# Optimization experiments

Hardware: AMD Instinct MI355X
Metric: run time of the kernel (lower is better)

## Reference

```python
import jax, jax.numpy as jnp
import numpy as np

B, L, ENC, EMB, H, V = 64, 33, 512, 256, 512, 32000


def setup_inputs() -> dict:
    key = jax.random.key(0)
    ks = jax.random.split(key, 16)
    x = jax.random.normal(ks[0], (B, ENC), dtype=jnp.float32)
    padded_target = jax.random.randint(ks[1], (B, L), 0, V)
    target_lengths = jax.random.randint(ks[2], (B,), 2, L + 1)
    target_lengths = target_lengths.at[0].set(L)  # pin max length -> static step count
    s = 0.05
    return {
        "x": x,
        "padded_target": padded_target,
        "target_lengths": target_lengths,
        "embed": jax.random.normal(ks[3], (V, EMB), dtype=jnp.float32) * s,
        "W_h0": jax.random.normal(ks[4], (H, ENC), dtype=jnp.float32) * s,
        "b_h0": jnp.zeros((H,), jnp.float32),
        "W_c0": jax.random.normal(ks[5], (H, ENC), dtype=jnp.float32) * s,
        "b_c0": jnp.zeros((H,), jnp.float32),
        "W_ih": jax.random.normal(ks[6], (4 * H, ENC + EMB), dtype=jnp.float32) * s,
        "W_hh": jax.random.normal(ks[7], (4 * H, H), dtype=jnp.float32) * s,
        "b_ih": jnp.zeros((4 * H,), jnp.float32),
        "b_hh": jnp.zeros((4 * H,), jnp.float32),
        "W_out": jax.random.normal(ks[8], (V, H), dtype=jnp.float32) * s,
        "b_out": jnp.zeros((V,), jnp.float32),
    }


def reference(x, padded_target, target_lengths, embed, W_h0, b_h0, W_c0, b_c0,
              W_ih, W_hh, b_ih, b_hh, W_out, b_out):
    # sort by length, descending (packed-sequence ordering)
    sorted_indices = jnp.argsort(-target_lengths)
    x = x[sorted_indices]                      # [B, ENC]
    tgt = padded_target[sorted_indices]        # [B, L]
    lens = target_lengths[sorted_indices] - 1  # decode steps per row
    emb = embed[tgt]                           # [B, L, EMB]

    h = x @ W_h0.T + b_h0                      # context-initialized state
    c = x @ W_c0.T + b_c0
    T = padded_target.shape[1] - 1             # static max steps (max len pinned to L)

    def step(carry, inp):
        h, c = carry
        e_t, t = inp
        active = (lens > t)[:, None]           # rows still decoding (prefix, sorted)
        g = jnp.concatenate([x, e_t], axis=1) @ W_ih.T + b_ih + h @ W_hh.T + b_hh
        i, f, gg, o = jnp.split(g, 4, axis=1)  # torch LSTMCell gate order i,f,g,o
        c_new = jax.nn.sigmoid(f) * c + jax.nn.sigmoid(i) * jnp.tanh(gg)
        h_new = jax.nn.sigmoid(o) * jnp.tanh(c_new)
        h = jnp.where(active, h_new, h)        # inactive rows keep frozen state
        c = jnp.where(active, c_new, c)
        pred = jnp.where(active, h_new @ W_out.T + b_out, 0.0)  # dropout p=0
        return (h, c), pred

    (_, _), preds = jax.lax.scan(
        step, (h, c), (jnp.transpose(emb[:, :T], (1, 0, 2)), jnp.arange(T)))
    prediction = jnp.transpose(preds, (1, 0, 2))  # [B, T, V]
    return prediction, sorted_indices
```

## Files before the change

kernel.cpp:

```cpp
#include <hip/hip_runtime.h>

typedef __attribute__((ext_vector_type(8))) short short8;
typedef __attribute__((ext_vector_type(8))) unsigned short ushort8;
typedef __attribute__((ext_vector_type(4))) float f32x4;

#define DEV __device__ __forceinline__

DEV unsigned short f2bf(float f) {
  unsigned int u = __float_as_uint(f);
  u += 0x7fffu + ((u >> 16) & 1u);
  return (unsigned short)(u >> 16);
}
DEV float sigm(float x) { return 1.f / (1.f + __expf(-x)); }
DEV float tanh_(float x) { return 1.f - 2.f / (1.f + __expf(2.f * x)); }

typedef __attribute__((address_space(1))) const void* as1cv;
typedef __attribute__((address_space(3))) void* as3v;
DEV void gll16(const void* g, void* l) {
  __builtin_amdgcn_global_load_lds((as1cv)g, (as3v)l, 16, 0, 0);
}

__global__ void __launch_bounds__(256) k_pre(const float* __restrict__ x,
    const int* __restrict__ ptar, const int* __restrict__ tlen,
    const float* __restrict__ W_h0, const float* __restrict__ W_c0,
    const float* __restrict__ W_ih, const float* __restrict__ W_hh,
    int* __restrict__ sidx, int* __restrict__ lens, int* __restrict__ base,
    int* __restrict__ inv, int* __restrict__ Pw, int* __restrict__ tok,
    unsigned short* __restrict__ xsb, float* __restrict__ tail,
    unsigned short* __restrict__ Wpro, unsigned short* __restrict__ Wihb2,
    unsigned short* __restrict__ Whb) {
  int bid = blockIdx.x, tid = threadIdx.x;
  if (bid > 0) {
    long long g = (long long)(bid - 1) * 2048 + tid * 8;
    const float* src;
    unsigned short* dst;
    if (g < 262144) {
      src = W_h0 + g; dst = Wpro + g;
    } else if (g < 524288) {
      long long l = g - 262144; src = W_c0 + l; dst = Wpro + 262144 + l;
    } else if (g < 1572864) {
      long long l = g - 524288;
      long long r = l >> 9, c = l & 511;
      src = W_ih + r * 768 + c; dst = Wpro + 524288 + l;
    } else if (g < 2097152) {
      long long l = g - 1572864;
      long long r = l >> 8, c = l & 255;
      src = W_ih + r * 768 + 512 + c; dst = Wihb2 + l;
    } else {
      long long l = g - 2097152; src = W_hh + l; dst = Whb + l;
    }
    float4 v0 = *(const float4*)src, v1 = *(const float4*)(src + 4);
    ushort8 o;
    o[0] = f2bf(v0.x); o[1] = f2bf(v0.y); o[2] = f2bf(v0.z); o[3] = f2bf(v0.w);
    o[4] = f2bf(v1.x); o[5] = f2bf(v1.y); o[6] = f2bf(v1.z); o[7] = f2bf(v1.w);
    *(ushort8*)dst = o;
    return;
  }
  __shared__ int ss[64], ls[64], bs[64];
  if (tid < 64) {
    int li = tlen[tid];
    int rank = 0;
    for (int j = 0; j < 64; ++j) {
      int lj = tlen[j];
      rank += (lj > li || (lj == li && j < tid)) ? 1 : 0;
    }
    ss[rank] = tid;
  }
  __syncthreads();
  if (tid < 64) {
    int src = ss[tid];
    sidx[tid] = src;
    int l = tlen[src] - 1;
    ls[tid] = l;
    lens[tid] = l;
    tail[tid] = (float)src;
  }
  __syncthreads();
  if (tid == 0) {
    int s = 0;
    for (int b = 0; b < 64; ++b) { bs[b] = s; base[b] = s; s += ls[b]; }
    Pw[0] = s;
  }
  __syncthreads();
  for (int idx = tid; idx < 2048; idx += 256) {
    int b = idx >> 5, t = idx & 31;
    if (t < ls[b]) inv[bs[b] + t] = idx;
  }
  for (int idx = tid; idx < 32 * 64; idx += 256) {
    int t = idx >> 6, b = idx & 63;
    tok[idx] = ptar[ss[b] * 33 + t];
  }
  for (int idx = tid; idx < 64 * 512; idx += 256) {
    int b = idx >> 9;
    xsb[idx] = f2bf(x[ss[b] * 512 + (idx & 511)]);
  }
}

__global__ void __launch_bounds__(256) k_mid(const unsigned short* __restrict__ xsb,
    const unsigned short* __restrict__ Wpro, const float* __restrict__ b_h0,
    const float* __restrict__ b_c0, const float* __restrict__ b_ih,
    const float* __restrict__ b_hh, unsigned short* __restrict__ h0b,
    float* __restrict__ c, float* __restrict__ gx,
    const int* __restrict__ tok, const float* __restrict__ embed,
    unsigned short* __restrict__ Eb) {
  int bid = blockIdx.x, tid = threadIdx.x;
  if (bid >= 48) {
    int gid = (bid - 48) * 256 + tid;
    int row = gid >> 5, c8 = (gid & 31) * 8;
    const float* src = embed + (size_t)tok[row] * 256 + c8;
    float4 v0 = *(const float4*)src, v1 = *(const float4*)(src + 4);
    ushort8 o;
    o[0] = f2bf(v0.x); o[1] = f2bf(v0.y); o[2] = f2bf(v0.z); o[3] = f2bf(v0.w);
    o[4] = f2bf(v1.x); o[5] = f2bf(v1.y); o[6] = f2bf(v1.z); o[7] = f2bf(v1.w);
    *(ushort8*)(Eb + (size_t)row * 256 + c8) = o;
    return;
  }
  int lane = tid & 63, w = tid >> 6;
  int n0 = bid * 64 + w * 16;
  int lr = lane & 15, lk = lane >> 4;
  f32x4 acc[4];
#pragma unroll
  for (int i = 0; i < 4; ++i) acc[i] = (f32x4){0.f, 0.f, 0.f, 0.f};
  const unsigned short* B = Wpro + (size_t)(n0 + lr) * 512 + lk * 8;
  const unsigned short* A = xsb + (size_t)lr * 512 + lk * 8;
#pragma unroll
  for (int ks = 0; ks < 16; ++ks) {
    short8 bfr = *(const short8*)(B + ks * 32);
#pragma unroll
    for (int mi = 0; mi < 4; ++mi) {
      short8 af = *(const short8*)(A + mi * 16 * 512 + ks * 32);
      acc[mi] = __builtin_amdgcn_mfma_f32_16x16x32_bf16(af, bfr, acc[mi], 0, 0, 0);
    }
  }
  int n = n0 + lr;
#pragma unroll
  for (int mi = 0; mi < 4; ++mi)
#pragma unroll
    for (int r = 0; r < 4; ++r) {
      int b = mi * 16 + lk * 4 + r;
      float v = acc[mi][r];
      if (n < 512) {
        h0b[b * 512 + n] = f2bf(v + b_h0[n]);
      } else if (n < 1024) {
        int u = n - 512;
        c[b * 512 + u] = v + b_c0[u];
      } else {
        int j = n - 1024;
        gx[(size_t)b * 2048 + j] = v + b_ih[j] + b_hh[j];
      }
    }
}

__global__ void __launch_bounds__(256) k_ga2(const unsigned short* __restrict__ Eb,
    const unsigned short* __restrict__ Wb2, const float* __restrict__ gx,
    float* __restrict__ GA, const float* __restrict__ W_out,
    unsigned short* __restrict__ Wob) {
  int bid = blockIdx.x, tid = threadIdx.x;
  if (bid >= 256) {
    long long basei = (long long)(bid - 256) * 65536;
#pragma unroll 4
    for (int it = 0; it < 32; ++it) {
      long long i = basei + (long long)it * 2048 + tid * 8;
      float4 v0 = *(const float4*)(W_out + i);
      float4 v1 = *(const float4*)(W_out + i + 4);
      ushort8 o;
      o[0] = f2bf(v0.x); o[1] = f2bf(v0.y); o[2] = f2bf(v0.z); o[3] = f2bf(v0.w);
      o[4] = f2bf(v1.x); o[5] = f2bf(v1.y); o[6] = f2bf(v1.z); o[7] = f2bf(v1.w);
      *(ushort8*)(Wob + i) = o;
    }
    return;
  }
  __shared__ alignas(16) char ldsbuf[32768];
  char* ldsA = ldsbuf;
  char* ldsB = ldsbuf + 16384;
  int mt = bid & 15, nt = bid >> 4;
  int m0 = mt * 128, n0 = nt * 128;
  int lane = tid & 63, w = tid >> 6;
  int wm = w >> 1, wn = w & 1;
  f32x4 acc[4][4];
#pragma unroll
  for (int a = 0; a < 4; ++a)
#pragma unroll
    for (int bq = 0; bq < 4; ++bq) acc[a][bq] = (f32x4){0.f, 0.f, 0.f, 0.f};
  const unsigned short* Arow = Eb + (size_t)m0 * 256;
  const unsigned short* Brow = Wb2 + (size_t)n0 * 256;
  for (int kt = 0; kt < 4; ++kt) {
    int k0 = kt * 64;
    if (kt) __syncthreads();
#pragma unroll
    for (int j = 0; j < 4; ++j) {
      int ci = j * 256 + w * 64 + lane;
      int r = ci >> 3;
      int clog = ((ci & 7) << 4) ^ ((r & 7) << 4);
      int ldst = (j * 256 + w * 64) * 16;
      gll16((const char*)(Arow + (size_t)r * 256 + k0) + clog, ldsA + ldst);
      gll16((const char*)(Brow + (size_t)r * 256 + k0) + clog, ldsB + ldst);
    }
    __syncthreads();
#pragma unroll
    for (int kk = 0; kk < 2; ++kk) {
      short8 af[4], bf[4];
      int cb = kk * 64 + (lane >> 4) * 16;
#pragma unroll
      for (int i = 0; i < 4; ++i) {
        int ar = wm * 64 + i * 16 + (lane & 15);
        af[i] = *(const short8*)(ldsA + ar * 128 + (cb ^ ((ar & 7) << 4)));
        int br = wn * 64 + i * 16 + (lane & 15);
        bf[i] = *(const short8*)(ldsB + br * 128 + (cb ^ ((br & 7) << 4)));
      }
#pragma unroll
      for (int mi = 0; mi < 4; ++mi)
#pragma unroll
        for (int ni = 0; ni < 4; ++ni)
          acc[mi][ni] = __builtin_amdgcn_mfma_f32_16x16x32_bf16(
              af[mi], bf[ni], acc[mi][ni], 0, 0, 0);
    }
  }
#pragma unroll
  for (int mi = 0; mi < 4; ++mi) {
    int mb = m0 + wm * 64 + mi * 16 + ((lane >> 4) << 2);
#pragma unroll
    for (int r = 0; r < 4; ++r) {
      int m = mb + r;
#pragma unroll
      for (int ni = 0; ni < 4; ++ni) {
        int j = n0 + wn * 64 + ni * 16 + (lane & 15);
        GA[(size_t)m * 2048 + j] = acc[mi][ni][r] + gx[(size_t)(m & 63) * 2048 + j];
      }
    }
  }
}

__global__ void __launch_bounds__(256, 1) k_step4(
    const unsigned short* __restrict__ hin, unsigned short* __restrict__ hout,
    float* __restrict__ c, const float* __restrict__ GA,
    const unsigned short* __restrict__ Whb, const int* __restrict__ lens,
    const int* __restrict__ base, unsigned short* __restrict__ Hm, int t) {
  int tid = threadIdx.x, bid = blockIdx.x;
  int mq = bid & 3, ug = bid >> 2;
  int r0 = mq * 16;
  if (t > lens[r0]) return;
  int lane = tid & 63, w = tid >> 6;
  int lr = lane & 15, lk = lane >> 4;
  int gate = lr >> 2, ul = lr & 3;
  int u = ug * 16 + w * 4 + ul;

  const float* gab = GA + ((size_t)t * 64 + r0) * 2048 + gate * 512 + u;
  float gv[4];
#pragma unroll
  for (int r = 0; r < 4; ++r) gv[r] = gab[(size_t)(lk * 4 + r) * 2048];

  const unsigned short* Bp = Whb + ((size_t)gate * 512 + u) * 512 + lk * 8;
  const unsigned short* Ap = hin + (size_t)(r0 + lr) * 512 + lk * 8;
  short8 bfr[16], afr[16];
#pragma unroll
  for (int ks = 0; ks < 16; ++ks) bfr[ks] = *(const short8*)(Bp + ks * 32);
#pragma unroll
  for (int ks = 0; ks < 16; ++ks) afr[ks] = *(const short8*)(Ap + ks * 32);
  f32x4 acc = (f32x4){0.f, 0.f, 0.f, 0.f};
#pragma unroll
  for (int ks = 0; ks < 16; ++ks)
    acc = __builtin_amdgcn_mfma_f32_16x16x32_bf16(afr[ks], bfr[ks], acc, 0, 0, 0);

#pragma unroll
  for (int r = 0; r < 4; ++r) {
    float v = acc[r] + gv[r];
    float av = (gate == 2) ? tanh_(v) : sigm(v);
    float x4 = __shfl_xor(av, 4);
    float x8 = __shfl_xor(av, 8);
    float x12 = __shfl_xor(av, 12);
    float vi = (gate == 0) ? av : (gate == 1) ? x4 : (gate == 2) ? x8 : x12;
    float vf = (gate == 1) ? av : (gate == 0) ? x4 : (gate == 3) ? x8 : x12;
    float vg = (gate == 2) ? av : (gate == 3) ? x4 : (gate == 0) ? x8 : x12;
    float vo = (gate == 3) ? av : (gate == 2) ? x4 : (gate == 1) ? x8 : x12;
    if (gate == 0) {
      int b = r0 + lk * 4 + r;
      float cold = c[b * 512 + u];
      float cn = vf * cold + vi * vg;
      float hn = vo * tanh_(cn);
      bool act = lens[b] > t;
      if (act) c[b * 512 + u] = cn;
      unsigned short hbv = f2bf(hn);
      hout[b * 512 + u] = act ? hbv : hin[b * 512 + u];
      if (act) Hm[((size_t)(base[b] + t)) * 512 + u] = hbv;
    }
  }
}

__global__ void __launch_bounds__(512) k_gemm(const unsigned short* __restrict__ Hm,
    const unsigned short* __restrict__ Wb, const float* __restrict__ b_out,
    const int* __restrict__ inv, const int* __restrict__ Pw,
    const int* __restrict__ lens, float* __restrict__ out) {
  int bid = blockIdx.x, tid = threadIdx.x;
  if (bid >= 2000) {
    int idx = bid - 2000;
    float4 z = {0.f, 0.f, 0.f, 0.f};
#pragma unroll
    for (int k = 0; k < 4; ++k) {
      int m = idx * 4 + k;
      int b = m >> 5, t = m & 31;
      if (lens[b] > t) continue;
      float* row = out + (size_t)m * 32000;
      for (int i = tid * 4; i < 32000; i += 2048) *(float4*)(row + i) = z;
    }
    return;
  }
  __shared__ alignas(16) char ldsbuf[49152];
  char* ldsA = ldsbuf;
  char* ldsB = ldsbuf + 16384;
  int P = Pw[0];
  int sb = (bid & 7) * 250 + (bid >> 3);
  int mt = sb % 16, nt = sb / 16;
  int m0 = mt * 128, n0 = nt * 256;
  if (m0 >= P) return;
  int lane = tid & 63, w = tid >> 6;
  int wm = w >> 2, wn = w & 3;
  f32x4 acc[4][4];
#pragma unroll
  for (int a = 0; a < 4; ++a)
#pragma unroll
    for (int bq = 0; bq < 4; ++bq) acc[a][bq] = (f32x4){0.f, 0.f, 0.f, 0.f};
  const unsigned short* Arow = Hm + (size_t)m0 * 512;
  const unsigned short* Brow = Wb + (size_t)n0 * 512;
  for (int kt = 0; kt < 8; ++kt) {
    int k0 = kt * 64;
    if (kt) __syncthreads();
#pragma unroll
    for (int j = 0; j < 2; ++j) {
      int ci = j * 512 + tid;
      int r = ci >> 3;
      int clog = ((ci & 7) << 4) ^ ((r & 7) << 4);
      gll16((const char*)(Arow + (size_t)r * 512 + k0) + clog, ldsA + ci * 16);
    }
#pragma unroll
    for (int j = 0; j < 4; ++j) {
      int ci = j * 512 + tid;
      int r = ci >> 3;
      int clog = ((ci & 7) << 4) ^ ((r & 7) << 4);
      gll16((const char*)(Brow + (size_t)r * 512 + k0) + clog, ldsB + ci * 16);
    }
    __syncthreads();
#pragma unroll
    for (int kk = 0; kk < 2; ++kk) {
      short8 af[4], bf[4];
      int cb = kk * 64 + (lane >> 4) * 16;
#pragma unroll
      for (int i = 0; i < 4; ++i) {
        int ar = wm * 64 + i * 16 + (lane & 15);
        af[i] = *(const short8*)(ldsA + ar * 128 + (cb ^ ((ar & 7) << 4)));
        int br = wn * 64 + i * 16 + (lane & 15);
        bf[i] = *(const short8*)(ldsB + br * 128 + (cb ^ ((br & 7) << 4)));
      }
#pragma unroll
      for (int mi = 0; mi < 4; ++mi)
#pragma unroll
        for (int ni = 0; ni < 4; ++ni)
          acc[mi][ni] = __builtin_amdgcn_mfma_f32_16x16x32_bf16(
              af[mi], bf[ni], acc[mi][ni], 0, 0, 0);
    }
  }
#pragma unroll
  for (int mi = 0; mi < 4; ++mi) {
    int pb = m0 + wm * 64 + mi * 16 + ((lane >> 4) << 2);
#pragma unroll
    for (int r = 0; r < 4; ++r) {
      int p = pb + r;
      if (p >= P) continue;
      size_t orow = (size_t)inv[p] * 32000;
#pragma unroll
      for (int ni = 0; ni < 4; ++ni) {
        int n = n0 + wn * 64 + ni * 16 + (lane & 15);
        out[orow + n] = acc[mi][ni][r] + b_out[n];
      }
    }
  }
}

extern "C" void kernel_launch(void* const* d_in, const int* in_sizes, int n_in,
                              void* d_out, int out_size, void* d_ws, size_t ws_size,
                              hipStream_t stream) {
  const float* x     = (const float*)d_in[0];
  const int*   ptar  = (const int*)d_in[1];
  const int*   tlen  = (const int*)d_in[2];
  const float* embed = (const float*)d_in[3];
  const float* W_h0  = (const float*)d_in[4];
  const float* b_h0  = (const float*)d_in[5];
  const float* W_c0  = (const float*)d_in[6];
  const float* b_c0  = (const float*)d_in[7];
  const float* W_ih  = (const float*)d_in[8];
  const float* W_hh  = (const float*)d_in[9];
  const float* b_ih  = (const float*)d_in[10];
  const float* b_hh  = (const float*)d_in[11];
  const float* W_out = (const float*)d_in[12];
  const float* b_out = (const float*)d_in[13];
  float* out = (float*)d_out;

  char* ws = (char*)d_ws;
  size_t off = 0;
  auto alloc = [&](size_t bytes) {
    void* p = ws + off;
    off += (bytes + 255) & ~(size_t)255;
    return p;
  };
  unsigned short* Wob = (unsigned short*)alloc(32000ull * 512 * 2);
  unsigned short* Hm  = (unsigned short*)alloc(2048ull * 512 * 2);
  unsigned short* h0b = (unsigned short*)alloc(64 * 512 * 2);
  unsigned short* h1b = (unsigned short*)alloc(64 * 512 * 2);
  float* cbuf = (float*)alloc(64 * 512 * 4);
  float* gx   = (float*)alloc(64 * 2048 * 4);
  int* sidx = (int*)alloc(64 * 4);
  int* lens = (int*)alloc(64 * 4);
  int* base = (int*)alloc(64 * 4);
  int* inv  = (int*)alloc(2048 * 4);
  int* Pw   = (int*)alloc(4);
  int* tok  = (int*)alloc(2048 * 4);

  float* GA = out;
  unsigned short* Wpro  = (unsigned short*)(out + 4194304);
  unsigned short* Wihb2 = (unsigned short*)(out + 4980736);
  unsigned short* Whb   = (unsigned short*)(out + 5242880);
  unsigned short* Eb    = (unsigned short*)(out + 5767168);
  unsigned short* xsb   = (unsigned short*)(out + 6029312);
  float* tail = out + 65536000;

  k_pre<<<1537, 256, 0, stream>>>(x, ptar, tlen, W_h0, W_c0, W_ih, W_hh,
                                  sidx, lens, base, inv, Pw, tok, xsb, tail,
                                  Wpro, Wihb2, Whb);
  k_mid<<<304, 256, 0, stream>>>(xsb, Wpro, b_h0, b_c0, b_ih, b_hh, h0b, cbuf,
                                 gx, tok, embed, Eb);
  k_ga2<<<506, 256, 0, stream>>>(Eb, Wihb2, gx, GA, W_out, Wob);

  unsigned short* hb[2] = {h0b, h1b};
  for (int t = 0; t < 32; ++t)
    k_step4<<<128, 256, 0, stream>>>(hb[t & 1], hb[(t + 1) & 1], cbuf, GA, Whb,
                                     lens, base, Hm, t);

  k_gemm<<<2512, 512, 0, stream>>>(Hm, Wob, b_out, inv, Pw, lens, out);
  (void)in_sizes; (void)n_in; (void)out_size; (void)ws_size;
}
```

Baseline: 433.3 us.

## Fuse LSTM step launches into persistent kernel with global atomic barriers

Replaces the 32 per-timestep k_step4 launches with one persistent k_steps kernel that keeps W_hh fragments, cell state and the previous h in registers. Blocks in the same 16-row group synchronise each step through an atomic counter barrier, with h exchanged through cache-bypassing loads and stores. The next step's gate inputs are prefetched, and the W_out bf16 conversion moves from k_ga2 into extra blocks of the step kernel so it overlaps the serial recurrence. The barrier depends on all 32 blocks of a row group being co-resident, which is a deadlock risk, and the spin loop can contend with the conversion blocks for bandwidth.

```diff
diff --git a/kernel.cpp b/kernel.cpp
--- a/kernel.cpp
+++ b/kernel.cpp
@@ -18,6 +18,18 @@
 typedef __attribute__((address_space(3))) void* as3v;
 DEV void gll16(const void* g, void* l) {
   __builtin_amdgcn_global_load_lds((as1cv)g, (as3v)l, 16, 0, 0);
+}
+
+DEV void st2_llc(unsigned short* p, unsigned short v) {
+  unsigned int vv = v;
+  asm volatile("global_store_short %0, %1, off sc0 sc1" :: "v"(p), "v"(vv)
+               : "memory");
+}
+DEV short8 ld16_llc(const unsigned short* p) {
+  short8 r;
+  asm volatile("global_load_dwordx4 %0, %1, off sc0 sc1" : "=&v"(r) : "v"(p)
+               : "memory");
+  return r;
 }
 
 __global__ void __launch_bounds__(256) k_pre(const float* __restrict__ x,
@@ -28,7 +40,7 @@
     int* __restrict__ inv, int* __restrict__ Pw, int* __restrict__ tok,
     unsigned short* __restrict__ xsb, float* __restrict__ tail,
     unsigned short* __restrict__ Wpro, unsigned short* __restrict__ Wihb2,
-    unsigned short* __restrict__ Whb) {
+    unsigned short* __restrict__ Whb, int* __restrict__ bar) {
   int bid = blockIdx.x, tid = threadIdx.x;
   if (bid > 0) {
     long long g = (long long)(bid - 1) * 2048 + tid * 8;
@@ -57,6 +69,7 @@
     return;
   }
   __shared__ int ss[64], ls[64], bs[64];
+  for (int idx = tid; idx < 2048; idx += 256) bar[idx] = 0;
   if (tid < 64) {
     int li = tlen[tid];
     int rank = 0;
@@ -153,26 +166,11 @@
 
 __global__ void __launch_bounds__(256) k_ga2(const unsigned short* __restrict__ Eb,
     const unsigned short* __restrict__ Wb2, const float* __restrict__ gx,
-    float* __restrict__ GA, const float* __restrict__ W_out,
-    unsigned short* __restrict__ Wob) {
-  int bid = blockIdx.x, tid = threadIdx.x;
-  if (bid >= 256) {
-    long long basei = (long long)(bid - 256) * 65536;
-#pragma unroll 4
-    for (int it = 0; it < 32; ++it) {
-      long long i = basei + (long long)it * 2048 + tid * 8;
-      float4 v0 = *(const float4*)(W_out + i);
-      float4 v1 = *(const float4*)(W_out + i + 4);
-      ushort8 o;
-      o[0] = f2bf(v0.x); o[1] = f2bf(v0.y); o[2] = f2bf(v0.z); o[3] = f2bf(v0.w);
-      o[4] = f2bf(v1.x); o[5] = f2bf(v1.y); o[6] = f2bf(v1.z); o[7] = f2bf(v1.w);
-      *(ushort8*)(Wob + i) = o;
-    }
-    return;
-  }
+    float* __restrict__ GA) {
   __shared__ alignas(16) char ldsbuf[32768];
   char* ldsA = ldsbuf;
   char* ldsB = ldsbuf + 16384;
+  int bid = blockIdx.x, tid = threadIdx.x;
   int mt = bid & 15, nt = bid >> 4;
   int m0 = mt * 128, n0 = nt * 128;
   int lane = tid & 63, w = tid >> 6;
@@ -231,58 +229,115 @@
   }
 }
 
-__global__ void __launch_bounds__(256, 1) k_step4(
-    const unsigned short* __restrict__ hin, unsigned short* __restrict__ hout,
-    float* __restrict__ c, const float* __restrict__ GA,
+__global__ void __launch_bounds__(256, 1) k_steps(
+    unsigned short* __restrict__ h0, unsigned short* __restrict__ h1,
+    const float* __restrict__ c0, const float* __restrict__ GA,
     const unsigned short* __restrict__ Whb, const int* __restrict__ lens,
-    const int* __restrict__ base, unsigned short* __restrict__ Hm, int t) {
+    const int* __restrict__ base, unsigned short* __restrict__ Hm,
+    int* __restrict__ bar, const float* __restrict__ W_out,
+    unsigned short* __restrict__ Wob) {
   int tid = threadIdx.x, bid = blockIdx.x;
+  if (bid >= 128) {
+    for (long long i = ((long long)(bid - 128) * 256 + tid) * 8; i < 16384000LL;
+         i += 128LL * 256 * 8) {
+      float4 v0 = *(const float4*)(W_out + i);
+      float4 v1 = *(const float4*)(W_out + i + 4);
+      ushort8 o;
+      o[0] = f2bf(v0.x); o[1] = f2bf(v0.y); o[2] = f2bf(v0.z); o[3] = f2bf(v0.w);
+      o[4] = f2bf(v1.x); o[5] = f2bf(v1.y); o[6] = f2bf(v1.z); o[7] = f2bf(v1.w);
+      *(ushort8*)(Wob + i) = o;
+    }
+    return;
+  }
+  int lane = tid & 63, w = tid >> 6;
+  int lr = lane & 15, lk = lane >> 4;
   int mq = bid & 3, ug = bid >> 2;
   int r0 = mq * 16;
-  if (t > lens[r0]) return;
-  int lane = tid & 63, w = tid >> 6;
-  int lr = lane & 15, lk = lane >> 4;
   int gate = lr >> 2, ul = lr & 3;
   int u = ug * 16 + w * 4 + ul;
-
-  const float* gab = GA + ((size_t)t * 64 + r0) * 2048 + gate * 512 + u;
+  int L0 = lens[r0];
+
+  short8 bfr[16];
+  {
+    const unsigned short* Bp = Whb + ((size_t)gate * 512 + u) * 512 + lk * 8;
+#pragma unroll
+    for (int ks = 0; ks < 16; ++ks) bfr[ks] = *(const short8*)(Bp + ks * 32);
+  }
+  float cr[4];
+  unsigned short hprev[4];
+#pragma unroll
+  for (int r = 0; r < 4; ++r) {
+    int b = r0 + lk * 4 + r;
+    cr[r] = c0[b * 512 + u];
+    hprev[r] = h0[b * 512 + u];
+  }
   float gv[4];
-#pragma unroll
-  for (int r = 0; r < 4; ++r) gv[r] = gab[(size_t)(lk * 4 + r) * 2048];
-
-  const unsigned short* Bp = Whb + ((size_t)gate * 512 + u) * 512 + lk * 8;
-  const unsigned short* Ap = hin + (size_t)(r0 + lr) * 512 + lk * 8;
-  short8 bfr[16], afr[16];
-#pragma unroll
-  for (int ks = 0; ks < 16; ++ks) bfr[ks] = *(const short8*)(Bp + ks * 32);
-#pragma unroll
-  for (int ks = 0; ks < 16; ++ks) afr[ks] = *(const short8*)(Ap + ks * 32);
-  f32x4 acc = (f32x4){0.f, 0.f, 0.f, 0.f};
-#pragma unroll
-  for (int ks = 0; ks < 16; ++ks)
-    acc = __builtin_amdgcn_mfma_f32_16x16x32_bf16(afr[ks], bfr[ks], acc, 0, 0, 0);
-
-#pragma unroll
-  for (int r = 0; r < 4; ++r) {
-    float v = acc[r] + gv[r];
-    float av = (gate == 2) ? tanh_(v) : sigm(v);
-    float x4 = __shfl_xor(av, 4);
-    float x8 = __shfl_xor(av, 8);
-    float x12 = __shfl_xor(av, 12);
-    float vi = (gate == 0) ? av : (gate == 1) ? x4 : (gate == 2) ? x8 : x12;
-    float vf = (gate == 1) ? av : (gate == 0) ? x4 : (gate == 3) ? x8 : x12;
-    float vg = (gate == 2) ? av : (gate == 3) ? x4 : (gate == 0) ? x8 : x12;
-    float vo = (gate == 3) ? av : (gate == 2) ? x4 : (gate == 1) ? x8 : x12;
-    if (gate == 0) {
-      int b = r0 + lk * 4 + r;
-      float cold = c[b * 512 + u];
-      float cn = vf * cold + vi * vg;
-      float hn = vo * tanh_(cn);
-      bool act = lens[b] > t;
-      if (act) c[b * 512 + u] = cn;
-      unsigned short hbv = f2bf(hn);
-      hout[b * 512 + u] = act ? hbv : hin[b * 512 + u];
-      if (act) Hm[((size_t)(base[b] + t)) * 512 + u] = hbv;
+  {
+    const float* gab = GA + (size_t)r0 * 2048 + gate * 512 + u;
+#pragma unroll
+    for (int r = 0; r < 4; ++r) gv[r] = gab[(size_t)(lk * 4 + r) * 2048];
+  }
+
+  for (int t = 0; t < L0; ++t) {
+    const unsigned short* hin = (t & 1) ? h1 : h0;
+    unsigned short* hout = (t & 1) ? h0 : h1;
+    const unsigned short* Ap = hin + (size_t)(r0 + lr) * 512 + lk * 8;
+    short8 afr[16];
+#pragma unroll
+    for (int ks = 0; ks < 16; ++ks) afr[ks] = ld16_llc(Ap + ks * 32);
+    asm volatile("s_waitcnt vmcnt(0)" ::: "memory");
+    __builtin_amdgcn_sched_barrier(0);
+    f32x4 acc = (f32x4){0.f, 0.f, 0.f, 0.f};
+#pragma unroll
+    for (int ks = 0; ks < 16; ++ks)
+      acc = __builtin_amdgcn_mfma_f32_16x16x32_bf16(afr[ks], bfr[ks], acc, 0, 0, 0);
+
+    float gvn[4] = {0.f, 0.f, 0.f, 0.f};
+    if (t + 1 < 32) {
+      const float* gabn = GA + ((size_t)(t + 1) * 64 + r0) * 2048 + gate * 512 + u;
+#pragma unroll
+      for (int r = 0; r < 4; ++r) gvn[r] = gabn[(size_t)(lk * 4 + r) * 2048];
+    }
+
+#pragma unroll
+    for (int r = 0; r < 4; ++r) {
+      float v = acc[r] + gv[r];
+      float av = (gate == 2) ? tanh_(v) : sigm(v);
+      float x4 = __shfl_xor(av, 4);
+      float x8 = __shfl_xor(av, 8);
+      float x12 = __shfl_xor(av, 12);
+      float vi = (gate == 0) ? av : (gate == 1) ? x4 : (gate == 2) ? x8 : x12;
+      float vf = (gate == 1) ? av : (gate == 0) ? x4 : (gate == 3) ? x8 : x12;
+      float vg = (gate == 2) ? av : (gate == 3) ? x4 : (gate == 0) ? x8 : x12;
+      float vo = (gate == 3) ? av : (gate == 2) ? x4 : (gate == 1) ? x8 : x12;
+      if (gate == 0) {
+        int b = r0 + lk * 4 + r;
+        float cn = vf * cr[r] + vi * vg;
+        float hn = vo * tanh_(cn);
+        bool act = lens[b] > t;
+        if (act) cr[r] = cn;
+        unsigned short hbv = f2bf(hn);
+        unsigned short hw = act ? hbv : hprev[r];
+        st2_llc(hout + b * 512 + u, hw);
+        hprev[r] = hw;
+        if (act) Hm[((size_t)(base[b] + t)) * 512 + u] = hbv;
+      }
+    }
+#pragma unroll
+    for (int r = 0; r < 4; ++r) gv[r] = gvn[r];
+
+    if (t + 1 < L0) {
+      asm volatile("s_waitcnt vmcnt(0)" ::: "memory");
+      __syncthreads();
+      if (tid == 0) {
+        int* ctr = bar + (mq * 32 + t) * 16;
+        __hip_atomic_fetch_add(ctr, 1, __ATOMIC_RELAXED,
+                               __HIP_MEMORY_SCOPE_AGENT);
+        while (__hip_atomic_load(ctr, __ATOMIC_RELAXED,
+                                 __HIP_MEMORY_SCOPE_AGENT) < 32)
+          __builtin_amdgcn_s_sleep(2);
+      }
+      __syncthreads();
     }
   }
 }
@@ -414,6 +469,7 @@
   int* inv  = (int*)alloc(2048 * 4);
   int* Pw   = (int*)alloc(4);
   int* tok  = (int*)alloc(2048 * 4);
+  int* bar  = (int*)alloc(2048 * 4);
 
   float* GA = out;
   unsigned short* Wpro  = (unsigned short*)(out + 4194304);
@@ -425,16 +481,12 @@
 
   k_pre<<<1537, 256, 0, stream>>>(x, ptar, tlen, W_h0, W_c0, W_ih, W_hh,
                                   sidx, lens, base, inv, Pw, tok, xsb, tail,
-                                  Wpro, Wihb2, Whb);
+                                  Wpro, Wihb2, Whb, bar);
   k_mid<<<304, 256, 0, stream>>>(xsb, Wpro, b_h0, b_c0, b_ih, b_hh, h0b, cbuf,
                                  gx, tok, embed, Eb);
-  k_ga2<<<506, 256, 0, stream>>>(Eb, Wihb2, gx, GA, W_out, Wob);
-
-  unsigned short* hb[2] = {h0b, h1b};
-  for (int t = 0; t < 32; ++t)
-    k_step4<<<128, 256, 0, stream>>>(hb[t & 1], hb[(t + 1) & 1], cbuf, GA, Whb,
-                                     lens, base, Hm, t);
-
+  k_ga2<<<256, 256, 0, stream>>>(Eb, Wihb2, gx, GA);
+  k_steps<<<256, 256, 0, stream>>>(h0b, h1b, cbuf, GA, Whb, lens, base, Hm,
+                                   bar, W_out, Wob);
   k_gemm<<<2512, 512, 0, stream>>>(Hm, Wob, b_out, inv, Pw, lens, out);
   (void)in_sizes; (void)n_in; (void)out_size; (void)ws_size;
 }
```

New measurement: 380.1 us. -12.3%, faster.
